# Performance work log

Hardware: AMD Instinct MI355X
Metric: run time of the kernel (lower is better)

The kernel has to match this reference:

```python
import jax, jax.numpy as jnp
import numpy as np

NEG_SLOPE = 0.2


def _gat_conv(x, src, dst, W, a_l, a_r, b, n_nodes, activate):
    """DGL-style GATConv. x:[N,F_in], W:[F_in,H*D], a_l/a_r/b:[H,D]."""
    H, D = a_l.shape
    feat = (x @ W).reshape(n_nodes, H, D)                      # [N,H,D]
    el = jnp.sum(feat * a_l, axis=-1)                          # [N,H]
    er = jnp.sum(feat * a_r, axis=-1)                          # [N,H]
    e = jax.nn.leaky_relu(el[src] + er[dst], NEG_SLOPE)        # [E,H]
    # edge softmax over incoming edges of each dst node (numerically stable)
    emax = jax.ops.segment_max(e, dst, num_segments=n_nodes)   # [N,H]
    emax = jnp.where(jnp.isfinite(emax), emax, 0.0)            # zero-in-degree safe
    ee = jnp.exp(e - emax[dst])                                # [E,H]
    denom = jax.ops.segment_sum(ee, dst, num_segments=n_nodes) # [N,H]
    alpha = ee / jnp.maximum(denom[dst], 1e-9)                 # [E,H]
    # aggregate alpha-weighted src features into dst
    msg = alpha[:, :, None] * feat[src]                        # [E,H,D]
    out = jax.ops.segment_sum(msg, dst, num_segments=n_nodes)  # [N,H,D]
    out = out + b
    if activate:
        out = jax.nn.elu(out)
    return out


def setup_inputs() -> dict:
    key = jax.random.key(0)
    ks = jax.random.split(key, 16)
    N, E, F_in, H, Dh, C = 50000, 800000, 256, 4, 64, 40
    s = lambda fan_in: 1.0 / np.sqrt(fan_in)
    return {
        "x": jax.random.normal(ks[0], (N, F_in), dtype=jnp.float32),
        "edge_index": jax.random.randint(ks[1], (2, E), 0, N, dtype=jnp.int32),
        "W0": jax.random.normal(ks[2], (F_in, H * Dh), dtype=jnp.float32) * s(F_in),
        "al0": jax.random.normal(ks[3], (H, Dh), dtype=jnp.float32) * s(Dh),
        "ar0": jax.random.normal(ks[4], (H, Dh), dtype=jnp.float32) * s(Dh),
        "b0": jnp.zeros((H, Dh), dtype=jnp.float32),
        "W1": jax.random.normal(ks[5], (H * Dh, H * Dh), dtype=jnp.float32) * s(H * Dh),
        "al1": jax.random.normal(ks[6], (H, Dh), dtype=jnp.float32) * s(Dh),
        "ar1": jax.random.normal(ks[7], (H, Dh), dtype=jnp.float32) * s(Dh),
        "b1": jnp.zeros((H, Dh), dtype=jnp.float32),
        "W2": jax.random.normal(ks[8], (H * Dh, H * C), dtype=jnp.float32) * s(H * Dh),
        "al2": jax.random.normal(ks[9], (H, C), dtype=jnp.float32) * s(C),
        "ar2": jax.random.normal(ks[10], (H, C), dtype=jnp.float32) * s(C),
        "b2": jnp.zeros((H, C), dtype=jnp.float32),
    }


def reference(x, edge_index, W0, al0, ar0, b0, W1, al1, ar1, b1, W2, al2, ar2, b2):
    N = x.shape[0]
    src, dst = edge_index[0], edge_index[1]
    h = _gat_conv(x, src, dst, W0, al0, ar0, b0, N, activate=True).reshape(N, -1)
    h = _gat_conv(h, src, dst, W1, al1, ar1, b1, N, activate=True).reshape(N, -1)
    out = _gat_conv(h, src, dst, W2, al2, ar2, b2, N, activate=False)
    logits = out.mean(axis=1)  # mean over heads -> [N, num_classes]
    return logits
```

## Files before the change

### kernel.cpp

```cpp
#include <hip/hip_runtime.h>
#include <hip/hip_bf16.h>
#include <math.h>

#define NEG_SLOPE 0.2f

typedef unsigned short ushortT;
typedef __attribute__((ext_vector_type(8))) short short8;
typedef __attribute__((ext_vector_type(4))) float f32x4;
typedef __attribute__((ext_vector_type(4), aligned(4))) int   int4u;

static __device__ __forceinline__ float leaky(float x){ return x > 0.f ? x : NEG_SLOPE * x; }
static __device__ __forceinline__ float elu(float x){ return x > 0.f ? x : (__expf(x) - 1.f); }

static __device__ __forceinline__ ushortT f2bf(float f){
  unsigned u = __float_as_uint(f);
  u += 0x7fff + ((u >> 16) & 1);
  return (ushortT)(u >> 16);
}
static __device__ __forceinline__ float bf2f(ushortT h){ return __uint_as_float((unsigned)h << 16); }
static __device__ __forceinline__ float bf_lo(unsigned u){ return __uint_as_float(u << 16); }
static __device__ __forceinline__ float bf_hi(unsigned u){ return __uint_as_float(u & 0xffff0000u); }


__global__ void hist_kernel(const int* __restrict__ dst, int E, int* __restrict__ counts){
  int i = blockIdx.x*blockDim.x + threadIdx.x;
  if(i < E) atomicAdd(&counts[dst[i]], 1);
}

__global__ void scan1_kernel(const int* __restrict__ counts, int N,
                             int* __restrict__ offsets, int* __restrict__ blocksums){
  __shared__ int sdata[1024];
  int i = blockIdx.x*1024 + threadIdx.x;
  int v = (i<N) ? counts[i] : 0;
  sdata[threadIdx.x] = v;
  __syncthreads();
  for(int off=1; off<1024; off<<=1){
    int t = (threadIdx.x >= off) ? sdata[threadIdx.x-off] : 0;
    __syncthreads();
    sdata[threadIdx.x] += t;
    __syncthreads();
  }
  if(i<N) offsets[i] = sdata[threadIdx.x] - v;
  if(threadIdx.x==1023) blocksums[blockIdx.x] = sdata[1023];
}

__global__ void scan3_kernel(int* __restrict__ offsets, const int* __restrict__ blocksums,
                             int N, int E, int* __restrict__ cursor){
  __shared__ int sbase;
  if(threadIdx.x == 0){
    int s = 0;
    for(int i=0;i<(int)blockIdx.x;i++) s += blocksums[i];
    sbase = s;
  }
  __syncthreads();
  int i = blockIdx.x*1024 + threadIdx.x;
  if(i < N){
    int o = offsets[i] + sbase;
    offsets[i] = o;
    cursor[i] = o;
  }
  if(i == 0) offsets[N] = E;
}

__global__ void scatter_kernel(const int* __restrict__ src, const int* __restrict__ dst, int E,
                               int* __restrict__ cursor, int* __restrict__ ssrc){
  int i = blockIdx.x*blockDim.x + threadIdx.x;
  if(i < E){
    int d = dst[i];
    int p = atomicAdd(&cursor[d], 1);
    ssrc[p] = src[i];
  }
}

__global__ __launch_bounds__(256) void pack_all(
    const float* __restrict__ x, int M, int Mpad, int xblocks,
    ushortT* __restrict__ Xh, ushortT* __restrict__ Xl,
    const float* __restrict__ W0, const float* __restrict__ W1, const float* __restrict__ W2,
    ushortT* __restrict__ Wph0, ushortT* __restrict__ Wpl0,
    ushortT* __restrict__ Wph1, ushortT* __restrict__ Wpl1,
    ushortT* __restrict__ Wph2, ushortT* __restrict__ Wpl2){
  int b = blockIdx.x;
  if(b < xblocks){
    int idx = b*256 + threadIdx.x;
    if(idx >= 8*Mpad) return;
    int t = idx / Mpad, m = idx - t*Mpad;
    size_t base = (size_t)idx * 32;
    if(m < M){
      const float* xr = &x[(size_t)m*256 + t*32];
      #pragma unroll
      for(int c=0;c<4;c++){
        float4 v0 = *(const float4*)&xr[c*8];
        float4 v1 = *(const float4*)&xr[c*8+4];
        float vv[8] = {v0.x,v0.y,v0.z,v0.w,v1.x,v1.y,v1.z,v1.w};
        ushortT h[8], l[8];
        #pragma unroll
        for(int j=0;j<8;j++){
          h[j] = f2bf(vv[j]);
          l[j] = f2bf(vv[j] - bf2f(h[j]));
        }
        *(short8*)&Xh[base + c*8] = *(short8*)h;
        *(short8*)&Xl[base + c*8] = *(short8*)l;
      }
    } else {
      short8 z = {0,0,0,0,0,0,0,0};
      #pragma unroll
      for(int c=0;c<4;c++){ *(short8*)&Xh[base + c*8] = z; *(short8*)&Xl[base + c*8] = z; }
    }
  } else {
    int wb = b - xblocks;
    int which = wb >> 5;
    const float* W = (which==0) ? W0 : (which==1) ? W1 : W2;
    ushortT* Wh = (which==0) ? Wph0 : (which==1) ? Wph1 : Wph2;
    ushortT* Wl = (which==0) ? Wpl0 : (which==1) ? Wpl1 : Wpl2;
    int Nn = (which==2) ? 160 : 256;
    int idx = (wb & 31)*256 + threadIdx.x;
    int lane = idx & 63;
    int t  = (idx >> 6) & 7;
    int nt = idx >> 9;
    int l15 = lane & 15, quad = lane >> 4;
    int n = nt*16 + l15;
    ushortT h[8], l[8];
    #pragma unroll
    for(int j=0;j<8;j++){
      int k = t*32 + quad*8 + j;
      float v = (n < Nn) ? W[(size_t)k*Nn + n] : 0.f;
      h[j] = f2bf(v);
      l[j] = f2bf(v - bf2f(h[j]));
    }
    *(short8*)&Wh[(size_t)idx*8] = *(short8*)h;
    *(short8*)&Wl[(size_t)idx*8] = *(short8*)l;
  }
}

__global__ __launch_bounds__(256) void gemm_packed(
    const ushortT* __restrict__ Ah, const ushortT* __restrict__ Al,
    const ushortT* __restrict__ Bh, const ushortT* __restrict__ Bl,
    ushortT* __restrict__ Cm, int M, int Mpad, int N, int ntiles,
    const float* __restrict__ al, const float* __restrict__ ar,
    float* __restrict__ el, float* __restrict__ er){
  __shared__ ushortT sAh[8192];
  __shared__ ushortT sAl[8192];
  const int tid  = threadIdx.x;
  const int lane = tid & 63;
  const int wv   = tid >> 6;
  const int l15  = lane & 15, quad = lane >> 4;
  const int m0   = blockIdx.x*32;
  const int n0   = wv*64;
  const int nt0  = n0 >> 4;

  {
    const short8* gh = (const short8*)Ah;
    const short8* gl = (const short8*)Al;
    short8* sh = (short8*)sAh;
    short8* sl = (short8*)sAl;
    #pragma unroll
    for(int c0=0;c0<4;c0++){
      int c = c0*256 + tid;
      int t = c >> 7;
      int rem = c & 127;
      size_t g = ((size_t)t*Mpad + m0)*4 + rem;
      sh[c] = gh[g];
      sl[c] = gl[g];
    }
  }
  __syncthreads();

  f32x4 acc[2][4];
  #pragma unroll
  for(int i=0;i<2;i++)
    #pragma unroll
    for(int j=0;j<4;j++){ acc[i][j][0]=0.f; acc[i][j][1]=0.f; acc[i][j][2]=0.f; acc[i][j][3]=0.f; }

  const short8* sh8 = (const short8*)sAh;
  const short8* sl8 = (const short8*)sAl;
  const short8* bh8 = (const short8*)Bh;
  const short8* bl8 = (const short8*)Bl;

  #pragma unroll
  for(int t=0; t<8; t++){
    short8 a_h[2], a_l[2], b_h[4], b_l[4];
    #pragma unroll
    for(int i=0;i<2;i++){
      int ci = t*128 + (i*16 + l15)*4 + quad;
      a_h[i] = sh8[ci];
      a_l[i] = sl8[ci];
    }
    #pragma unroll
    for(int j=0;j<4;j++){
      if(nt0 + j < ntiles){
        size_t bd = (((size_t)(nt0+j)*8 + t)*64 + lane);
        b_h[j] = bh8[bd];
        b_l[j] = bl8[bd];
      }
    }
    #pragma unroll
    for(int i=0;i<2;i++)
      #pragma unroll
      for(int j=0;j<4;j++){
        if(nt0 + j < ntiles){
          acc[i][j] = __builtin_amdgcn_mfma_f32_16x16x32_bf16(a_h[i], b_h[j], acc[i][j], 0,0,0);
          acc[i][j] = __builtin_amdgcn_mfma_f32_16x16x32_bf16(a_h[i], b_l[j], acc[i][j], 0,0,0);
          acc[i][j] = __builtin_amdgcn_mfma_f32_16x16x32_bf16(a_l[i], b_h[j], acc[i][j], 0,0,0);
        }
      }
  }

  if(al){
    const int h = wv;
    float alv[4], arv[4];
    #pragma unroll
    for(int j=0;j<4;j++){
      alv[j] = al[h*64 + j*16 + l15];
      arv[j] = ar[h*64 + j*16 + l15];
    }
    #pragma unroll
    for(int i=0;i<2;i++){
      #pragma unroll
      for(int r=0;r<4;r++){
        float pl = acc[i][0][r]*alv[0] + acc[i][1][r]*alv[1]
                 + acc[i][2][r]*alv[2] + acc[i][3][r]*alv[3];
        float pr = acc[i][0][r]*arv[0] + acc[i][1][r]*arv[1]
                 + acc[i][2][r]*arv[2] + acc[i][3][r]*arv[3];
        #pragma unroll
        for(int off=1; off<16; off<<=1){ pl += __shfl_xor(pl,off); pr += __shfl_xor(pr,off); }
        int gm = m0 + i*16 + quad*4 + r;
        if(l15==0 && gm < M){ el[gm*4+h] = pl; er[gm*4+h] = pr; }
      }
    }
  }

  #pragma unroll
  for(int i=0;i<2;i++){
    #pragma unroll
    for(int r=0;r<4;r++){
      int gm = m0 + i*16 + quad*4 + r;
      if(gm >= M) continue;
      #pragma unroll
      for(int j=0;j<4;j++){
        int gn = n0 + j*16 + l15;
        if(gn < N) Cm[(size_t)gm*N + gn] = f2bf(acc[i][j][r]);
      }
    }
  }
}

__global__ __launch_bounds__(256) void attn_proj_bf(const ushortT* __restrict__ feat,
                             const float* __restrict__ a_l, const float* __restrict__ a_r,
                             float* __restrict__ el, float* __restrict__ er, int N){
  int wv = threadIdx.x >> 6;
  int lane = threadIdx.x & 63;
  int n = blockIdx.x*4 + wv;
  if(n >= N) return;
  int h = lane >> 4, c = lane & 15;
  const unsigned* row = (const unsigned*)&feat[((size_t)n*4 + h)*40];
  const float2* alp = (const float2*)&a_l[h*40];
  const float2* arp = (const float2*)&a_r[h*40];
  unsigned u0 = row[c];
  float2 al0 = alp[c], ar0 = arp[c];
  float f0 = bf_lo(u0), f1 = bf_hi(u0);
  float vl = f0*al0.x + f1*al0.y;
  float vr = f0*ar0.x + f1*ar0.y;
  if(c < 4){
    unsigned u1 = row[16 + c];
    float2 al1 = alp[16 + c], ar1 = arp[16 + c];
    float g0 = bf_lo(u1), g1 = bf_hi(u1);
    vl += g0*al1.x + g1*al1.y;
    vr += g0*ar1.x + g1*ar1.y;
  }
  #pragma unroll
  for(int off=1; off<16; off<<=1){ vl += __shfl_xor(vl, off); vr += __shfl_xor(vr, off); }
  if(c == 0){ el[n*4+h] = vl; er[n*4+h] = vr; }
}

__global__ __launch_bounds__(256) void agg_kernel(const uint4* __restrict__ feat4,
                           const float* __restrict__ el, const float* __restrict__ er,
                           const int* __restrict__ offsets, const int* __restrict__ ssrc,
                           const float* __restrict__ bias,
                           ushortT* __restrict__ Hh, ushortT* __restrict__ Hl,
                           int N, int Mpad){
  int wvi  = threadIdx.x >> 6;
  int lane = threadIdx.x & 63;
  int n = blockIdx.x*4 + wvi;
  if(n >= N) return;
  const int slot = lane >> 5;
  const int wl   = lane & 31;
  const int head = wl >> 3;
  const float ern = er[n*4 + head];
  int e0 = offsets[n], e1 = offsets[n+1];
  float a0=0.f,a1=0.f,a2=0.f,a3=0.f,a4=0.f,a5=0.f,a6=0.f,a7=0.f;
  float den = 0.f;
  int e = e0;
  for(; e+7 < e1; e += 8){
    int4u sv = *(const int4u*)&ssrc[e + slot*4];
    #pragma unroll
    for(int i=0;i<4;i++){
      int s = sv[i];
      float w = __expf(leaky(el[s*4 + head] + ern));
      uint4 q = feat4[(size_t)s*32 + wl];
      a0 = fmaf(w, bf_lo(q.x), a0); a1 = fmaf(w, bf_hi(q.x), a1);
      a2 = fmaf(w, bf_lo(q.y), a2); a3 = fmaf(w, bf_hi(q.y), a3);
      a4 = fmaf(w, bf_lo(q.z), a4); a5 = fmaf(w, bf_hi(q.z), a5);
      a6 = fmaf(w, bf_lo(q.w), a6); a7 = fmaf(w, bf_hi(q.w), a7);
      den += w;
    }
  }
  for(; e < e1; e += 2){
    int ee = e + slot;
    int ec = (ee < e1) ? ee : (e1 - 1);
    int s = ssrc[ec];
    float w = (ee < e1) ? __expf(leaky(el[s*4 + head] + ern)) : 0.f;
    uint4 q = feat4[(size_t)s*32 + wl];
    a0 = fmaf(w, bf_lo(q.x), a0); a1 = fmaf(w, bf_hi(q.x), a1);
    a2 = fmaf(w, bf_lo(q.y), a2); a3 = fmaf(w, bf_hi(q.y), a3);
    a4 = fmaf(w, bf_lo(q.z), a4); a5 = fmaf(w, bf_hi(q.z), a5);
    a6 = fmaf(w, bf_lo(q.w), a6); a7 = fmaf(w, bf_hi(q.w), a7);
    den += w;
  }
  a0 += __shfl_xor(a0,32); a1 += __shfl_xor(a1,32);
  a2 += __shfl_xor(a2,32); a3 += __shfl_xor(a3,32);
  a4 += __shfl_xor(a4,32); a5 += __shfl_xor(a5,32);
  a6 += __shfl_xor(a6,32); a7 += __shfl_xor(a7,32);
  den += __shfl_xor(den,32);
  if(slot == 0){
    float inv = 1.f / fmaxf(den, 1e-9f);
    int k0 = wl*8;
    float4 b4a = *(const float4*)&bias[k0];
    float4 b4b = *(const float4*)&bias[k0+4];
    float o[8];
    o[0] = elu(a0*inv + b4a.x); o[1] = elu(a1*inv + b4a.y);
    o[2] = elu(a2*inv + b4a.z); o[3] = elu(a3*inv + b4a.w);
    o[4] = elu(a4*inv + b4b.x); o[5] = elu(a5*inv + b4b.y);
    o[6] = elu(a6*inv + b4b.z); o[7] = elu(a7*inv + b4b.w);
    ushortT hh[8], ll[8];
    #pragma unroll
    for(int j=0;j<8;j++){
      hh[j] = f2bf(o[j]);
      ll[j] = f2bf(o[j] - bf2f(hh[j]));
    }
    int t  = wl >> 2;
    int co = (wl & 3) * 8;
    size_t ad = ((size_t)t*Mpad + n)*32 + co;
    *(short8*)&Hh[ad] = *(short8*)hh;
    *(short8*)&Hl[ad] = *(short8*)ll;
  }
}

__global__ __launch_bounds__(256) void agg2_kernel(const uint4* __restrict__ feat4,
                            const float* __restrict__ el, const float* __restrict__ er,
                            const int* __restrict__ offsets, const int* __restrict__ ssrc,
                            const float* __restrict__ bias, float* __restrict__ logits,
                            int N){
  int wv = threadIdx.x >> 6;
  int lane = threadIdx.x & 63;
  int n = blockIdx.x*4 + wv;
  if(n >= N) return;
  const int slot = lane / 20;
  const int wl   = lane - slot*20;
  const int head = wl / 5;
  const float ern = er[n*4 + head];
  int e0 = offsets[n], e1 = offsets[n+1];
  float a0=0.f,a1=0.f,a2=0.f,a3=0.f,a4=0.f,a5=0.f,a6=0.f,a7=0.f;
  float den = 0.f;
  #pragma unroll 2
  for(int e = e0; e < e1; e += 3){
    int ee = e + ((slot < 3) ? slot : 2);
    int ec = (ee < e1) ? ee : (e1 - 1);
    int s = ssrc[ec];
    bool act = (slot < 3) && (ee < e1);
    float w = act ? __expf(leaky(el[s*4 + head] + ern)) : 0.f;
    uint4 q = feat4[(size_t)s*20 + wl];
    a0 = fmaf(w, bf_lo(q.x), a0); a1 = fmaf(w, bf_hi(q.x), a1);
    a2 = fmaf(w, bf_lo(q.y), a2); a3 = fmaf(w, bf_hi(q.y), a3);
    a4 = fmaf(w, bf_lo(q.z), a4); a5 = fmaf(w, bf_hi(q.z), a5);
    a6 = fmaf(w, bf_lo(q.w), a6); a7 = fmaf(w, bf_hi(q.w), a7);
    den += w;
  }
  {
    float t1, t2;
    t1 = __shfl(a0, lane+20); t2 = __shfl(a0, lane+40); a0 += t1 + t2;
    t1 = __shfl(a1, lane+20); t2 = __shfl(a1, lane+40); a1 += t1 + t2;
    t1 = __shfl(a2, lane+20); t2 = __shfl(a2, lane+40); a2 += t1 + t2;
    t1 = __shfl(a3, lane+20); t2 = __shfl(a3, lane+40); a3 += t1 + t2;
    t1 = __shfl(a4, lane+20); t2 = __shfl(a4, lane+40); a4 += t1 + t2;
    t1 = __shfl(a5, lane+20); t2 = __shfl(a5, lane+40); a5 += t1 + t2;
    t1 = __shfl(a6, lane+20); t2 = __shfl(a6, lane+40); a6 += t1 + t2;
    t1 = __shfl(a7, lane+20); t2 = __shfl(a7, lane+40); a7 += t1 + t2;
    t1 = __shfl(den, lane+20); t2 = __shfl(den, lane+40); den += t1 + t2;
  }
  if(slot == 0){
    float inv = 1.f / fmaxf(den, 1e-9f);
    float4 ba = *(const float4*)&bias[wl*8];
    float4 bb = *(const float4*)&bias[wl*8+4];
    float o[8];
    o[0] = a0*inv + ba.x; o[1] = a1*inv + ba.y; o[2] = a2*inv + ba.z; o[3] = a3*inv + ba.w;
    o[4] = a4*inv + bb.x; o[5] = a5*inv + bb.y; o[6] = a6*inv + bb.z; o[7] = a7*inv + bb.w;
    #pragma unroll
    for(int j=0;j<8;j++){
      float t = __shfl(o[j], lane+5);  o[j] += t;
      t       = __shfl(o[j], lane+10); o[j] += t;
    }
    if(wl < 5){
      float4 r0, r1;
      r0.x = 0.25f*o[0]; r0.y = 0.25f*o[1]; r0.z = 0.25f*o[2]; r0.w = 0.25f*o[3];
      r1.x = 0.25f*o[4]; r1.y = 0.25f*o[5]; r1.z = 0.25f*o[6]; r1.w = 0.25f*o[7];
      *(float4*)&logits[(size_t)n*40 + wl*8]     = r0;
      *(float4*)&logits[(size_t)n*40 + wl*8 + 4] = r1;
    }
  }
}

extern "C" void kernel_launch(void* const* d_in, const int* in_sizes, int n_in,
                              void* d_out, int out_size, void* d_ws, size_t ws_size,
                              hipStream_t stream){
  const float* x   = (const float*)d_in[0];
  const int*   eix = (const int*)  d_in[1];
  const float* W0  = (const float*)d_in[2];
  const float* al0 = (const float*)d_in[3];
  const float* ar0 = (const float*)d_in[4];
  const float* b0  = (const float*)d_in[5];
  const float* W1  = (const float*)d_in[6];
  const float* al1 = (const float*)d_in[7];
  const float* ar1 = (const float*)d_in[8];
  const float* b1  = (const float*)d_in[9];
  const float* W2  = (const float*)d_in[10];
  const float* al2 = (const float*)d_in[11];
  const float* ar2 = (const float*)d_in[12];
  const float* b2  = (const float*)d_in[13];
  float* logits = (float*)d_out;

  const int N = in_sizes[0] / 256;
  const int E = in_sizes[1] / 2;
  const int* src = eix;
  const int* dst = eix + E;
  const int nb = (N + 1023) / 1024;

  char* ws = (char*)d_ws;
  auto alloc = [&](size_t bytes)->char*{
    char* p = ws; ws += (bytes + 255) & ~(size_t)255; return p;
  };
  const int nblocksM = (N + 127)/128;
  const int Mpad = nblocksM * 128;
  const size_t apackElems = (size_t)Mpad * 256;
  int*   counts    = (int*)  alloc((size_t)N*4);
  int*   offsets   = (int*)  alloc((size_t)(N+1)*4);
  int*   cursor    = (int*)  alloc((size_t)N*4);
  int*   blocksums = (int*)  alloc((size_t)nb*4);
  int*   ssrc      = (int*)  alloc((size_t)E*4);
  __hip_bfloat16* bufF = (__hip_bfloat16*)alloc((size_t)N*256*2);
  ushortT* Hh      = (ushortT*)alloc(apackElems*2);
  ushortT* Hl      = (ushortT*)alloc(apackElems*2);
  float* el_buf    = (float*)alloc((size_t)N*4*4);
  float* er_buf    = (float*)alloc((size_t)N*4*4);
  ushortT* Wph0 = (ushortT*)alloc(16*8*64*8*2);
  ushortT* Wpl0 = (ushortT*)alloc(16*8*64*8*2);
  ushortT* Wph1 = (ushortT*)alloc(16*8*64*8*2);
  ushortT* Wpl1 = (ushortT*)alloc(16*8*64*8*2);
  ushortT* Wph2 = (ushortT*)alloc(16*8*64*8*2);
  ushortT* Wpl2 = (ushortT*)alloc(16*8*64*8*2);

  hipMemsetAsync(counts, 0, (size_t)N*4, stream);
  hist_kernel   <<<(E+255)/256, 256, 0, stream>>>(dst, E, counts);
  scan1_kernel  <<<nb, 1024, 0, stream>>>(counts, N, offsets, blocksums);
  scan3_kernel  <<<nb, 1024, 0, stream>>>(offsets, blocksums, N, E, cursor);
  scatter_kernel<<<(E+255)/256, 256, 0, stream>>>(src, dst, E, cursor, ssrc);

  int xblocks = (8*Mpad + 255)/256;
  pack_all<<<xblocks + 96, 256, 0, stream>>>(x, N, Mpad, xblocks, Hh, Hl,
                                             W0, W1, W2, Wph0, Wpl0, Wph1, Wpl1, Wph2, Wpl2);

  int ggBlocks = Mpad / 32;
  int aggGrid  = (N+3)/4;
  gemm_packed<<<ggBlocks, 256, 0, stream>>>(Hh, Hl, Wph0, Wpl0, (ushortT*)bufF, N, Mpad, 256, 16, al0, ar0, el_buf, er_buf);
  agg_kernel<<<aggGrid, 256, 0, stream>>>((const uint4*)bufF, el_buf, er_buf, offsets, ssrc, b0, Hh, Hl, N, Mpad);
  gemm_packed<<<ggBlocks, 256, 0, stream>>>(Hh, Hl, Wph1, Wpl1, (ushortT*)bufF, N, Mpad, 256, 16, al1, ar1, el_buf, er_buf);
  agg_kernel<<<aggGrid, 256, 0, stream>>>((const uint4*)bufF, el_buf, er_buf, offsets, ssrc, b1, Hh, Hl, N, Mpad);
  gemm_packed<<<ggBlocks, 256, 0, stream>>>(Hh, Hl, Wph2, Wpl2, (ushortT*)bufF, N, Mpad, 160, 10, nullptr, nullptr, nullptr, nullptr);
  attn_proj_bf<<<aggGrid, 256, 0, stream>>>((const ushortT*)bufF, al2, ar2, el_buf, er_buf, N);
  agg2_kernel<<<aggGrid, 256, 0, stream>>>((const uint4*)bufF, el_buf, er_buf, offsets, ssrc, b2, logits, N);
}
```

Before: 512.6 us.

## Schedule aggregation waves by descending in-degree via counting-sort permutation

Adds a counting sort of destination nodes by in-degree, highest degree first, through a histogram, a scan and a scatter. The three aggregation kernels then map each wave to perm[idx] rather than to the node index directly. High-degree nodes start early and blocks with similar trip counts are grouped, which targets load imbalance and tail effects. The cost is three extra small kernel launches plus a memset, and output writes and el/er reads become scattered instead of sequential.

```diff
diff --git a/kernel.cpp b/kernel.cpp
--- a/kernel.cpp
+++ b/kernel.cpp
@@ -69,6 +69,38 @@
     int d = dst[i];
     int p = atomicAdd(&cursor[d], 1);
     ssrc[p] = src[i];
+  }
+}
+
+__global__ void deg_hist_kernel(const int* __restrict__ counts, int N, int* __restrict__ dhist){
+  int i = blockIdx.x*blockDim.x + threadIdx.x;
+  if(i < N){
+    int d = counts[i]; if(d > 1023) d = 1023;
+    atomicAdd(&dhist[1023 - d], 1);
+  }
+}
+
+__global__ void deg_scan_kernel(const int* __restrict__ dhist, int* __restrict__ dcur){
+  __shared__ int sdata[1024];
+  int v = dhist[threadIdx.x];
+  sdata[threadIdx.x] = v;
+  __syncthreads();
+  for(int off=1; off<1024; off<<=1){
+    int t = (threadIdx.x >= off) ? sdata[threadIdx.x-off] : 0;
+    __syncthreads();
+    sdata[threadIdx.x] += t;
+    __syncthreads();
+  }
+  dcur[threadIdx.x] = sdata[threadIdx.x] - v;
+}
+
+__global__ void deg_scatter_kernel(const int* __restrict__ counts, int N,
+                                   int* __restrict__ dcur, int* __restrict__ perm){
+  int i = blockIdx.x*blockDim.x + threadIdx.x;
+  if(i < N){
+    int d = counts[i]; if(d > 1023) d = 1023;
+    int p = atomicAdd(&dcur[1023 - d], 1);
+    perm[p] = i;
   }
 }
 
@@ -275,13 +307,15 @@
 __global__ __launch_bounds__(256) void agg_kernel(const uint4* __restrict__ feat4,
                            const float* __restrict__ el, const float* __restrict__ er,
                            const int* __restrict__ offsets, const int* __restrict__ ssrc,
+                           const int* __restrict__ perm,
                            const float* __restrict__ bias,
                            ushortT* __restrict__ Hh, ushortT* __restrict__ Hl,
                            int N, int Mpad){
   int wvi  = threadIdx.x >> 6;
   int lane = threadIdx.x & 63;
-  int n = blockIdx.x*4 + wvi;
-  if(n >= N) return;
+  int idx = blockIdx.x*4 + wvi;
+  if(idx >= N) return;
+  int n = perm[idx];
   const int slot = lane >> 5;
   const int wl   = lane & 31;
   const int head = wl >> 3;
@@ -348,12 +382,14 @@
 __global__ __launch_bounds__(256) void agg2_kernel(const uint4* __restrict__ feat4,
                             const float* __restrict__ el, const float* __restrict__ er,
                             const int* __restrict__ offsets, const int* __restrict__ ssrc,
+                            const int* __restrict__ perm,
                             const float* __restrict__ bias, float* __restrict__ logits,
                             int N){
   int wv = threadIdx.x >> 6;
   int lane = threadIdx.x & 63;
-  int n = blockIdx.x*4 + wv;
-  if(n >= N) return;
+  int idx = blockIdx.x*4 + wv;
+  if(idx >= N) return;
+  int n = perm[idx];
   const int slot = lane / 20;
   const int wl   = lane - slot*20;
   const int head = wl / 5;
@@ -446,6 +482,9 @@
   int*   cursor    = (int*)  alloc((size_t)N*4);
   int*   blocksums = (int*)  alloc((size_t)nb*4);
   int*   ssrc      = (int*)  alloc((size_t)E*4);
+  int*   perm      = (int*)  alloc((size_t)N*4);
+  int*   dhist     = (int*)  alloc(1024*4);
+  int*   dcur      = (int*)  alloc(1024*4);
   __hip_bfloat16* bufF = (__hip_bfloat16*)alloc((size_t)N*256*2);
   ushortT* Hh      = (ushortT*)alloc(apackElems*2);
   ushortT* Hl      = (ushortT*)alloc(apackElems*2);
@@ -459,11 +498,16 @@
   ushortT* Wpl2 = (ushortT*)alloc(16*8*64*8*2);
 
   hipMemsetAsync(counts, 0, (size_t)N*4, stream);
+  hipMemsetAsync(dhist, 0, 1024*4, stream);
   hist_kernel   <<<(E+255)/256, 256, 0, stream>>>(dst, E, counts);
   scan1_kernel  <<<nb, 1024, 0, stream>>>(counts, N, offsets, blocksums);
   scan3_kernel  <<<nb, 1024, 0, stream>>>(offsets, blocksums, N, E, cursor);
   scatter_kernel<<<(E+255)/256, 256, 0, stream>>>(src, dst, E, cursor, ssrc);
 
+  deg_hist_kernel   <<<(N+255)/256, 256, 0, stream>>>(counts, N, dhist);
+  deg_scan_kernel   <<<1, 1024, 0, stream>>>(dhist, dcur);
+  deg_scatter_kernel<<<(N+255)/256, 256, 0, stream>>>(counts, N, dcur, perm);
+
   int xblocks = (8*Mpad + 255)/256;
   pack_all<<<xblocks + 96, 256, 0, stream>>>(x, N, Mpad, xblocks, Hh, Hl,
                                              W0, W1, W2, Wph0, Wpl0, Wph1, Wpl1, Wph2, Wpl2);
@@ -471,10 +515,10 @@
   int ggBlocks = Mpad / 32;
   int aggGrid  = (N+3)/4;
   gemm_packed<<<ggBlocks, 256, 0, stream>>>(Hh, Hl, Wph0, Wpl0, (ushortT*)bufF, N, Mpad, 256, 16, al0, ar0, el_buf, er_buf);
-  agg_kernel<<<aggGrid, 256, 0, stream>>>((const uint4*)bufF, el_buf, er_buf, offsets, ssrc, b0, Hh, Hl, N, Mpad);
+  agg_kernel<<<aggGrid, 256, 0, stream>>>((const uint4*)bufF, el_buf, er_buf, offsets, ssrc, perm, b0, Hh, Hl, N, Mpad);
   gemm_packed<<<ggBlocks, 256, 0, stream>>>(Hh, Hl, Wph1, Wpl1, (ushortT*)bufF, N, Mpad, 256, 16, al1, ar1, el_buf, er_buf);
-  agg_kernel<<<aggGrid, 256, 0, stream>>>((const uint4*)bufF, el_buf, er_buf, offsets, ssrc, b1, Hh, Hl, N, Mpad);
+  agg_kernel<<<aggGrid, 256, 0, stream>>>((const uint4*)bufF, el_buf, er_buf, offsets, ssrc, perm, b1, Hh, Hl, N, Mpad);
   gemm_packed<<<ggBlocks, 256, 0, stream>>>(Hh, Hl, Wph2, Wpl2, (ushortT*)bufF, N, Mpad, 160, 10, nullptr, nullptr, nullptr, nullptr);
   attn_proj_bf<<<aggGrid, 256, 0, stream>>>((const ushortT*)bufF, al2, ar2, el_buf, er_buf, N);
-  agg2_kernel<<<aggGrid, 256, 0, stream>>>((const uint4*)bufF, el_buf, er_buf, offsets, ssrc, b2, logits, N);
-}
+  agg2_kernel<<<aggGrid, 256, 0, stream>>>((const uint4*)bufF, el_buf, er_buf, offsets, ssrc, perm, b2, logits, N);
+}
```

New measurement: 799.5 us. 1.56x slower.
